# Performance work log

Measured on AMD Instinct MI355X. Metric: run time of the kernel, lower is better.

The kernel has to match this reference:

```python
import jax, jax.numpy as jnp
import numpy as np

N_NODES = 100000
N_EDGES = 600000
D = 128          # encoder_output_dim
H = 64           # mlp_edge_model_dim


def setup_inputs() -> dict:
    key = jax.random.key(0)
    k1, k2, k3, k4, k5, k6 = jax.random.split(key, 6)
    node_emb = jax.random.normal(k1, (N_NODES, D), dtype=jnp.float32)
    edge_index = jax.random.randint(k2, (2, N_EDGES), 0, N_NODES, dtype=jnp.int64)
    # MLP params (Linear(2D -> H), Linear(H -> 1)); scale ~ PyTorch default init
    s1 = 1.0 / np.sqrt(2 * D)
    s2 = 1.0 / np.sqrt(H)
    W1 = jax.random.uniform(k3, (2 * D, H), dtype=jnp.float32, minval=-s1, maxval=s1)
    b1 = jax.random.uniform(k4, (H,), dtype=jnp.float32, minval=-s1, maxval=s1)
    W2 = jax.random.uniform(k5, (H, 1), dtype=jnp.float32, minval=-s2, maxval=s2)
    b2 = jax.random.uniform(k6, (1,), dtype=jnp.float32, minval=-s2, maxval=s2)
    return {"node_emb": node_emb, "edge_index": edge_index,
            "W1": W1, "b1": b1, "W2": W2, "b2": b2}


def reference(node_emb, edge_index, W1, b1, W2, b2):
    src, dst = edge_index[0], edge_index[1]
    emb_src = node_emb[src]                      # [E, D] gather
    emb_dst = node_emb[dst]                      # [E, D] gather
    edge_emb = jnp.concatenate([emb_src, emb_dst], axis=1)  # [E, 2D]
    h = jax.nn.relu(edge_emb @ W1 + b1)          # [E, H]
    edge_logits = h @ W2 + b2                    # [E, 1]
    return edge_logits
```

## Files before the change

kernel.cpp:

```cpp
#include <hip/hip_runtime.h>
#include <hip/hip_fp16.h>

#define N_NODES 100000
#define N_EDGES 600000
#define DIM 128
#define HID 64
#define TILES_TOTAL (N_NODES / 16)

typedef __attribute__((ext_vector_type(8))) _Float16 half8;
typedef __attribute__((ext_vector_type(4))) float floatx4;

__global__ __launch_bounds__(256) void precompute_P(
    const float* __restrict__ node_emb,
    const float* __restrict__ W1,
    const float* __restrict__ b1,
    __half* __restrict__ P)
{
    __shared__ alignas(16) _Float16 W1T[128][136];
    const int tid = threadIdx.x;

    for (int i = tid; i < 128 * 16; i += 256) {
        const int c  = i >> 4;
        const int kb = (i & 15) * 8;
        half8 h;
#pragma unroll
        for (int j = 0; j < 8; j++) {
            const int k = kb + j;
            const float w = (c < HID) ? W1[k * HID + c]
                                      : W1[(DIM + k) * HID + (c - HID)];
            h[j] = (_Float16)w;
        }
        *(half8*)&W1T[c][kb] = h;
    }
    __syncthreads();

    const int wid  = tid >> 6;
    const int lane = tid & 63;
    const int lr   = lane & 15;
    const int kq   = (lane >> 4) * 8;

    half8 bfr[8][4];
#pragma unroll
    for (int nt = 0; nt < 8; nt++)
#pragma unroll
        for (int ks = 0; ks < 4; ks++)
            bfr[nt][ks] = *(const half8*)&W1T[nt * 16 + lr][ks * 32 + kq];

    float bias[8];
#pragma unroll
    for (int nt = 0; nt < 8; nt++) {
        const int col = nt * 16 + lr;
        bias[nt] = (col < HID) ? b1[col] : 0.f;
    }

    const int nwaves = (int)(gridDim.x * 4);
    const int gw     = (int)(blockIdx.x * 4 + wid);
    const int crow   = (lane >> 4) * 4;

    for (int t = gw; t < TILES_TOTAL; t += nwaves) {
        const float* arow = node_emb + (size_t)(t * 16 + lr) * DIM + kq;
        float4 a[4][2];
#pragma unroll
        for (int ks = 0; ks < 4; ks++) {
            a[ks][0] = *(const float4*)(arow + ks * 32);
            a[ks][1] = *(const float4*)(arow + ks * 32 + 4);
        }
        floatx4 acc[8];
#pragma unroll
        for (int nt = 0; nt < 8; nt++) acc[nt] = (floatx4){0.f, 0.f, 0.f, 0.f};
#pragma unroll
        for (int ks = 0; ks < 4; ks++) {
            half8 af;
            af[0] = (_Float16)a[ks][0].x; af[1] = (_Float16)a[ks][0].y;
            af[2] = (_Float16)a[ks][0].z; af[3] = (_Float16)a[ks][0].w;
            af[4] = (_Float16)a[ks][1].x; af[5] = (_Float16)a[ks][1].y;
            af[6] = (_Float16)a[ks][1].z; af[7] = (_Float16)a[ks][1].w;
#pragma unroll
            for (int nt = 0; nt < 8; nt++)
                acc[nt] = __builtin_amdgcn_mfma_f32_16x16x32_f16(af, bfr[nt][ks], acc[nt], 0, 0, 0);
        }
        __half* prow = P + (size_t)(t * 16) * 128;
#pragma unroll
        for (int nt = 0; nt < 8; nt++) {
            const int col = nt * 16 + lr;
#pragma unroll
            for (int i = 0; i < 4; i++)
                prow[(size_t)(crow + i) * 128 + col] = __float2half(acc[nt][i] + bias[nt]);
        }
    }
}

__device__ inline bool detect_int64(const int* e32) {
    int orv = 0;
#pragma unroll
    for (int k = 0; k < 8; k++) orv |= e32[2 * k + 1];
    return orv == 0;
}

__global__ __launch_bounds__(256) void edge_mlp(
    const __half* __restrict__ P,
    const void* __restrict__ eidx_raw,
    const float* __restrict__ W2,
    const float* __restrict__ b2,
    float* __restrict__ out)
{
    const int* e32 = (const int*)eidx_raw;
    const long long* e64 = (const long long*)eidx_raw;
    const bool is64 = detect_int64(e32);

    const int tid  = threadIdx.x;
    const int lane = tid & 63;
    const int sub  = lane >> 5;
    const int j2   = lane & 31;
    const float2 w2 = *(const float2*)(W2 + 2 * j2);
    const float b2v = b2[0];
    const __half2* P2 = (const __half2*)P;

    const int gwid   = (int)((blockIdx.x * blockDim.x + tid) >> 6);
    const int nwaves = (int)((gridDim.x * blockDim.x) >> 6);

    for (int base = gwid * 8; base < N_EDGES; base += nwaves * 8) {
        int s[4], d[4];
#pragma unroll
        for (int u = 0; u < 4; u++) {
            const int e = base + 2 * u + sub;
            if (is64) { s[u] = (int)e64[e]; d[u] = (int)e64[N_EDGES + e]; }
            else      { s[u] = e32[e];      d[u] = e32[N_EDGES + e]; }
        }
        __half2 av[4], bv[4];
#pragma unroll
        for (int u = 0; u < 4; u++) {
            av[u] = P2[(size_t)s[u] * 64 + j2];
            bv[u] = P2[(size_t)d[u] * 64 + 32 + j2];
        }
#pragma unroll
        for (int u = 0; u < 4; u++) {
            const float2 a = __half22float2(av[u]);
            const float2 b = __half22float2(bv[u]);
            float t = fmaxf(a.x + b.x, 0.f) * w2.x
                    + fmaxf(a.y + b.y, 0.f) * w2.y;
#pragma unroll
            for (int off = 16; off >= 1; off >>= 1)
                t += __shfl_xor(t, off, 64);
            const float o1 = __shfl(t, 32, 64);
            if (lane == 0)
                *(float2*)(out + base + 2 * u) = make_float2(t + b2v, o1 + b2v);
        }
    }
}

__global__ __launch_bounds__(256) void edge_mlp_direct(
    const float* __restrict__ node_emb,
    const void* __restrict__ eidx_raw,
    const float* __restrict__ W1,
    const float* __restrict__ b1,
    const float* __restrict__ W2,
    const float* __restrict__ b2,
    float* __restrict__ out)
{
    const int* e32 = (const int*)eidx_raw;
    const long long* e64 = (const long long*)eidx_raw;
    const bool is64 = detect_int64(e32);

    const int lane = threadIdx.x & 63;
    const float w2  = W2[lane];
    const float b2v = b2[0];
    const int gwid   = (int)((blockIdx.x * blockDim.x + threadIdx.x) >> 6);
    const int nwaves = (int)((gridDim.x * blockDim.x) >> 6);

    for (int e = gwid; e < N_EDGES; e += nwaves) {
        int s, d;
        if (is64) { s = (int)e64[e]; d = (int)e64[N_EDGES + e]; }
        else      { s = e32[e];      d = e32[N_EDGES + e]; }
        const float* es = node_emb + (size_t)s * DIM;
        const float* ed = node_emb + (size_t)d * DIM;
        float acc = b1[lane];
        for (int k = 0; k < DIM; k++) {
            acc += es[k] * W1[k * HID + lane];
            acc += ed[k] * W1[(DIM + k) * HID + lane];
        }
        float t = fmaxf(acc, 0.f) * w2;
#pragma unroll
        for (int off = 32; off >= 1; off >>= 1)
            t += __shfl_xor(t, off, 64);
        if (lane == 0) out[e] = t + b2v;
    }
}

extern "C" void kernel_launch(void* const* d_in, const int* in_sizes, int n_in,
                              void* d_out, int out_size, void* d_ws, size_t ws_size,
                              hipStream_t stream) {
    const float* node_emb = (const float*)d_in[0];
    const void*  eidx     = d_in[1];
    const float* W1       = (const float*)d_in[2];
    const float* b1       = (const float*)d_in[3];
    const float* W2       = (const float*)d_in[4];
    const float* b2       = (const float*)d_in[5];
    float* out = (float*)d_out;

    const size_t pbytes = (size_t)N_NODES * 128 * sizeof(__half);
    if (ws_size >= pbytes) {
        __half* P = (__half*)d_ws;
        precompute_P<<<512, 256, 0, stream>>>(node_emb, W1, b1, P);
        edge_mlp<<<2048, 256, 0, stream>>>(P, eidx, W2, b2, out);
    } else {
        edge_mlp_direct<<<4096, 256, 0, stream>>>(node_emb, eidx, W1, b1, W2, b2, out);
    }
}
```

Baseline: 59.81 us.

## Hoist W1 transpose into prep kernel, one tile per wave, wider P gathers

Moves the per-block fp16 transpose of W1 into a separate prep kernel that writes it once to workspace. precompute_P now launches one wave per 16-node tile and reads weight fragments straight from global memory instead of LDS. It swaps the MFMA operand order so each lane stores four contiguous halfs per row. The edge kernel gathers 8-byte half4 chunks with 16 lanes per edge and does add/relu in packed fp16, which cuts per-edge shuffle rounds. The cost is an extra launch, repeated global weight reads per wave, fp16 rounding in the add, and a fallback to the slow direct kernel when workspace is between sizes.

```diff
diff --git a/kernel.cpp b/kernel.cpp
--- a/kernel.cpp
+++ b/kernel.cpp
@@ -8,85 +8,75 @@
 #define TILES_TOTAL (N_NODES / 16)
 
 typedef __attribute__((ext_vector_type(8))) _Float16 half8;
+typedef __attribute__((ext_vector_type(4))) _Float16 half4v;
 typedef __attribute__((ext_vector_type(4))) float floatx4;
+
+__global__ __launch_bounds__(256) void prep_W(
+    const float* __restrict__ W1, __half* __restrict__ W1T)
+{
+    const int o = (int)(blockIdx.x * blockDim.x + threadIdx.x) * 2;
+    if (o >= 128 * 128) return;
+    const int c = o >> 7, k = o & 127;
+    float w0, w1;
+    if (c < HID) { w0 = W1[k * HID + c];           w1 = W1[(k + 1) * HID + c]; }
+    else         { w0 = W1[(DIM + k) * HID + c - HID]; w1 = W1[(DIM + k + 1) * HID + c - HID]; }
+    W1T[o]     = __float2half(w0);
+    W1T[o + 1] = __float2half(w1);
+}
 
 __global__ __launch_bounds__(256) void precompute_P(
     const float* __restrict__ node_emb,
-    const float* __restrict__ W1,
+    const __half* __restrict__ W1T,
     const float* __restrict__ b1,
     __half* __restrict__ P)
 {
-    __shared__ alignas(16) _Float16 W1T[128][136];
-    const int tid = threadIdx.x;
-
-    for (int i = tid; i < 128 * 16; i += 256) {
-        const int c  = i >> 4;
-        const int kb = (i & 15) * 8;
-        half8 h;
-#pragma unroll
-        for (int j = 0; j < 8; j++) {
-            const int k = kb + j;
-            const float w = (c < HID) ? W1[k * HID + c]
-                                      : W1[(DIM + k) * HID + (c - HID)];
-            h[j] = (_Float16)w;
-        }
-        *(half8*)&W1T[c][kb] = h;
-    }
-    __syncthreads();
-
-    const int wid  = tid >> 6;
+    const int tid  = (int)(blockIdx.x * blockDim.x + threadIdx.x);
+    const int t    = tid >> 6;
+    if (t >= TILES_TOTAL) return;
     const int lane = tid & 63;
     const int lr   = lane & 15;
-    const int kq   = (lane >> 4) * 8;
-
-    half8 bfr[8][4];
-#pragma unroll
-    for (int nt = 0; nt < 8; nt++)
-#pragma unroll
-        for (int ks = 0; ks < 4; ks++)
-            bfr[nt][ks] = *(const half8*)&W1T[nt * 16 + lr][ks * 32 + kq];
-
-    float bias[8];
+    const int q    = lane >> 4;
+    const int kq   = q * 8;
+
+    const float* arow = node_emb + (size_t)(t * 16 + lr) * DIM + kq;
+    float4 a[4][2];
+#pragma unroll
+    for (int ks = 0; ks < 4; ks++) {
+        a[ks][0] = *(const float4*)(arow + ks * 32);
+        a[ks][1] = *(const float4*)(arow + ks * 32 + 4);
+    }
+
+    floatx4 acc[8];
+#pragma unroll
+    for (int nt = 0; nt < 8; nt++) acc[nt] = (floatx4){0.f, 0.f, 0.f, 0.f};
+
+#pragma unroll
+    for (int ks = 0; ks < 4; ks++) {
+        half8 af;
+        af[0] = (_Float16)a[ks][0].x; af[1] = (_Float16)a[ks][0].y;
+        af[2] = (_Float16)a[ks][0].z; af[3] = (_Float16)a[ks][0].w;
+        af[4] = (_Float16)a[ks][1].x; af[5] = (_Float16)a[ks][1].y;
+        af[6] = (_Float16)a[ks][1].z; af[7] = (_Float16)a[ks][1].w;
+#pragma unroll
+        for (int nt = 0; nt < 8; nt++) {
+            const half8 wf = *(const half8*)(W1T + (size_t)(nt * 16 + lr) * 128 + ks * 32 + kq);
+            acc[nt] = __builtin_amdgcn_mfma_f32_16x16x32_f16(wf, af, acc[nt], 0, 0, 0);
+        }
+    }
+
+    __half* prow = P + (size_t)(t * 16 + lr) * 128;
 #pragma unroll
     for (int nt = 0; nt < 8; nt++) {
-        const int col = nt * 16 + lr;
-        bias[nt] = (col < HID) ? b1[col] : 0.f;
-    }
-
-    const int nwaves = (int)(gridDim.x * 4);
-    const int gw     = (int)(blockIdx.x * 4 + wid);
-    const int crow   = (lane >> 4) * 4;
-
-    for (int t = gw; t < TILES_TOTAL; t += nwaves) {
-        const float* arow = node_emb + (size_t)(t * 16 + lr) * DIM + kq;
-        float4 a[4][2];
-#pragma unroll
-        for (int ks = 0; ks < 4; ks++) {
-            a[ks][0] = *(const float4*)(arow + ks * 32);
-            a[ks][1] = *(const float4*)(arow + ks * 32 + 4);
-        }
-        floatx4 acc[8];
-#pragma unroll
-        for (int nt = 0; nt < 8; nt++) acc[nt] = (floatx4){0.f, 0.f, 0.f, 0.f};
-#pragma unroll
-        for (int ks = 0; ks < 4; ks++) {
-            half8 af;
-            af[0] = (_Float16)a[ks][0].x; af[1] = (_Float16)a[ks][0].y;
-            af[2] = (_Float16)a[ks][0].z; af[3] = (_Float16)a[ks][0].w;
-            af[4] = (_Float16)a[ks][1].x; af[5] = (_Float16)a[ks][1].y;
-            af[6] = (_Float16)a[ks][1].z; af[7] = (_Float16)a[ks][1].w;
-#pragma unroll
-            for (int nt = 0; nt < 8; nt++)
-                acc[nt] = __builtin_amdgcn_mfma_f32_16x16x32_f16(af, bfr[nt][ks], acc[nt], 0, 0, 0);
-        }
-        __half* prow = P + (size_t)(t * 16) * 128;
-#pragma unroll
-        for (int nt = 0; nt < 8; nt++) {
-            const int col = nt * 16 + lr;
-#pragma unroll
-            for (int i = 0; i < 4; i++)
-                prow[(size_t)(crow + i) * 128 + col] = __float2half(acc[nt][i] + bias[nt]);
-        }
+        const int c0 = nt * 16 + q * 4;
+        float v0 = acc[nt][0], v1 = acc[nt][1], v2 = acc[nt][2], v3 = acc[nt][3];
+        if (nt < 4) {
+            const float4 bs = *(const float4*)(b1 + c0);
+            v0 += bs.x; v1 += bs.y; v2 += bs.z; v3 += bs.w;
+        }
+        half4v h;
+        h[0] = (_Float16)v0; h[1] = (_Float16)v1;
+        h[2] = (_Float16)v2; h[3] = (_Float16)v3;
+        *(half4v*)(prow + c0) = h;
     }
 }
 
@@ -110,41 +100,40 @@
 
     const int tid  = threadIdx.x;
     const int lane = tid & 63;
-    const int sub  = lane >> 5;
-    const int j2   = lane & 31;
-    const float2 w2 = *(const float2*)(W2 + 2 * j2);
+    const int j    = lane & 15;
+    const int grp  = lane >> 4;
+    const float4 w2 = *(const float4*)(W2 + 4 * j);
     const float b2v = b2[0];
-    const __half2* P2 = (const __half2*)P;
 
     const int gwid   = (int)((blockIdx.x * blockDim.x + tid) >> 6);
     const int nwaves = (int)((gridDim.x * blockDim.x) >> 6);
 
-    for (int base = gwid * 8; base < N_EDGES; base += nwaves * 8) {
+    const half4v zero = {(_Float16)0, (_Float16)0, (_Float16)0, (_Float16)0};
+
+    for (int base = gwid * 16; base < N_EDGES; base += nwaves * 16) {
         int s[4], d[4];
 #pragma unroll
         for (int u = 0; u < 4; u++) {
-            const int e = base + 2 * u + sub;
+            const int e = base + 4 * u + grp;
             if (is64) { s[u] = (int)e64[e]; d[u] = (int)e64[N_EDGES + e]; }
             else      { s[u] = e32[e];      d[u] = e32[N_EDGES + e]; }
         }
-        __half2 av[4], bv[4];
+        half4v av[4], bv[4];
 #pragma unroll
         for (int u = 0; u < 4; u++) {
-            av[u] = P2[(size_t)s[u] * 64 + j2];
-            bv[u] = P2[(size_t)d[u] * 64 + 32 + j2];
+            av[u] = *(const half4v*)(P + (size_t)s[u] * 128 + 4 * j);
+            bv[u] = *(const half4v*)(P + (size_t)d[u] * 128 + 64 + 4 * j);
         }
 #pragma unroll
         for (int u = 0; u < 4; u++) {
-            const float2 a = __half22float2(av[u]);
-            const float2 b = __half22float2(bv[u]);
-            float t = fmaxf(a.x + b.x, 0.f) * w2.x
-                    + fmaxf(a.y + b.y, 0.f) * w2.y;
-#pragma unroll
-            for (int off = 16; off >= 1; off >>= 1)
-                t += __shfl_xor(t, off, 64);
-            const float o1 = __shfl(t, 32, 64);
-            if (lane == 0)
-                *(float2*)(out + base + 2 * u) = make_float2(t + b2v, o1 + b2v);
+            const half4v t = av[u] + bv[u];
+            const half4v r = __builtin_elementwise_max(t, zero);
+            float acc = (float)r[0] * w2.x + (float)r[1] * w2.y
+                      + (float)r[2] * w2.z + (float)r[3] * w2.w;
+#pragma unroll
+            for (int off = 8; off >= 1; off >>= 1)
+                acc += __shfl_xor(acc, off, 64);
+            if (j == 0) out[base + 4 * u + grp] = acc + b2v;
         }
     }
 }
@@ -198,11 +187,20 @@
     const float* b2       = (const float*)d_in[5];
     float* out = (float*)d_out;
 
-    const size_t pbytes = (size_t)N_NODES * 128 * sizeof(__half);
-    if (ws_size >= pbytes) {
+    const size_t pbytes   = (size_t)N_NODES * 128 * sizeof(__half);
+    const size_t wt_off   = 32u * 1024 * 1024;
+    const size_t need     = wt_off + 128 * 128 * sizeof(__half);
+
+    if (ws_size >= need) {
+        __half* P   = (__half*)d_ws;
+        __half* W1T = (__half*)((char*)d_ws + wt_off);
+        prep_W<<<32, 256, 0, stream>>>(W1, W1T);
+        precompute_P<<<(TILES_TOTAL * 64 + 255) / 256, 256, 0, stream>>>(node_emb, W1T, b1, P);
+        edge_mlp<<<2048, 256, 0, stream>>>(P, eidx, W2, b2, out);
+    } else if (ws_size >= pbytes) {
         __half* P = (__half*)d_ws;
-        precompute_P<<<512, 256, 0, stream>>>(node_emb, W1, b1, P);
-        edge_mlp<<<2048, 256, 0, stream>>>(P, eidx, W2, b2, out);
+        edge_mlp_direct<<<4096, 256, 0, stream>>>(node_emb, eidx, W1, b1, W2, b2, out);
+        (void)P;
     } else {
         edge_mlp_direct<<<4096, 256, 0, stream>>>(node_emb, eidx, W1, b1, W2, b2, out);
     }
```

Result: slower. 69.71 us (+16.6%).
